# Performance work log

Measured on AMD Instinct MI355X. Metric: run time of the kernel, lower is better.

Reference implementation:

```python
import math
import jax, jax.numpy as jnp
import numpy as np

L_MAX = 3
PADDED = (1, 1, 2, 3)            # padded_l_list
K_MAX_L = (128, 96, 64, 32)      # channel bounds per l
FEATS = (32, 32, 32, 32)         # k_max_l[l] - k_max_l[l+1]
N_ATOMS = 20000
N_EDGES = 80000
N_RADIAL = 32
HIDDEN = 128
EPS = 1e-6


def setup_inputs() -> dict:
    key = jax.random.key(0)
    ks = jax.random.split(key, 40)
    it = iter(range(40))
    nk = lambda: ks[next(it)]
    inp = {}
    inp['rb'] = jax.random.normal(nk(), (L_MAX + 1, N_EDGES, N_RADIAL), jnp.float32)
    for l in range(L_MAX + 1):
        inp[f'sh{l}'] = jax.random.normal(nk(), (N_EDGES, 2 * l + 1), jnp.float32)
    for l in range(L_MAX + 1):
        P = PADDED[l]
        inp[f'f{l}'] = jax.random.normal(nk(), (N_ATOMS, P + 1, P + 1, FEATS[l]), jnp.float32)
    for P in (1, 2, 3):
        n = (P + 1) ** 2
        inp[f'U{P}'] = jax.random.normal(nk(), (n, n), jnp.float32) / math.sqrt(n)
    inp['gammas'] = jnp.ones((L_MAX + 1, 32), jnp.float32)
    inp['Win'] = jax.random.normal(nk(), (L_MAX + 1, 32, 32), jnp.float32) / math.sqrt(32.0)
    inp['Wout'] = jax.random.normal(nk(), (L_MAX + 1, 32, 32), jnp.float32) / math.sqrt(32.0)
    inp['A'] = jax.random.normal(nk(), (L_MAX + 1, N_RADIAL, HIDDEN), jnp.float32) / math.sqrt(float(N_RADIAL))
    for l in range(L_MAX + 1):
        inp[f'B{l}'] = jax.random.normal(nk(), (HIDDEN, K_MAX_L[l]), jnp.float32) / math.sqrt(float(HIDDEN))
    inp['msg_scale'] = jnp.float32(0.5)
    inp['centers'] = jax.random.randint(nk(), (N_EDGES,), 0, N_ATOMS)
    inp['neighbors'] = jax.random.randint(nk(), (N_EDGES,), 0, N_ATOMS)
    return inp


def _forward(rb, shs, feats, Us, gammas, Win, Wout, A, Bs, msg_scale, centers, neighbors):
    n_atoms = feats[0].shape[0]
    # EquivariantRMSNorm (norm over uncoupled i,j indices per channel) + linear_in
    h = []
    for l in range(L_MAX + 1):
        f = feats[l]
        rms = jnp.sqrt(jnp.mean(f * f, axis=(1, 2), keepdims=True) + EPS)
        fn = (f / rms) * gammas[l]
        h.append(jnp.einsum('nijf,fg->nijg', fn, Win[l]))
    # per-l radial MLP: [E, n_radial] -> silu -> [E, k_max_l[l]]
    rbm = [jax.nn.silu(rb[l] @ A[l]) @ Bs[l] for l in range(L_MAX + 1)]
    # vector expansion [E, 2l+1, k_max_l[l]]
    vexp = [shs[l][:, :, None] * rbm[l][:, None, :] for l in range(L_MAX + 1)]
    # split channels into per-l groups, uncouple via CG matrix U
    unc = []
    for l in range(L_MAX + 1):
        lower = K_MAX_L[l + 1] if l < L_MAX else 0
        upper = K_MAX_L[l]
        group = [vexp[lp][:, :, lower:upper] for lp in range(l + 1)]
        P = PADDED[l]
        if len(group) < P + 1:
            group.append(jnp.zeros((N_EDGES, 2 * P + 1, upper - lower), group[0].dtype))
        stacked = jnp.concatenate(group, axis=1)  # [E, (P+1)^2, feat]
        u = jnp.einsum('pq,eqf->epf', Us[P], stacked)
        unc.append(u.reshape(N_EDGES, P + 1, P + 1, upper - lower))
    # gather -> per-l tensor product -> scatter-add -> linear_out -> residual
    out = []
    for l in range(L_MAX + 1):
        P = PADDED[l]
        msg = jnp.einsum('eijf,ejkf->eikf', unc[l], h[l][neighbors]) / math.sqrt(P + 1.0)
        pooled = jnp.zeros((n_atoms,) + msg.shape[1:], msg.dtype).at[centers].add(msg) * msg_scale
        out.append(feats[l] + jnp.einsum('nijf,fg->nijg', pooled, Wout[l]))
    return tuple(out)


def reference(rb, sh0, sh1, sh2, sh3, f0, f1, f2, f3, U1, U2, U3, gammas, Win, Wout, A, B0, B1, B2, B3, msg_scale, centers, neighbors):
    return _forward(rb, [sh0, sh1, sh2, sh3], [f0, f1, f2, f3], {1: U1, 2: U2, 3: U3}, gammas, Win, Wout, A, [B0, B1, B2, B3], msg_scale, centers, neighbors)
```

## Files before the change

kernel.cpp:

```cpp
#include <hip/hip_runtime.h>
#include <cstdint>

#define NA 20000
#define NE 80000

typedef __attribute__((ext_vector_type(8))) short short8;
typedef __attribute__((ext_vector_type(4))) float f32x4;
typedef unsigned short ushort_t;

constexpr int HOFFc[4]   = {0, 2560000, 5120000, 10880000};
constexpr int RBMOFFc[4] = {0, 128, 224, 288};

__device__ __forceinline__ ushort_t f2bf(float x) {
    union { float f; unsigned u; } v; v.f = x;
    unsigned r = v.u + 0x7fffu + ((v.u >> 16) & 1u);
    return (ushort_t)(r >> 16);
}
__device__ __forceinline__ float bf2f(ushort_t u) {
    union { unsigned u; float f; } v; v.u = ((unsigned)u) << 16;
    return v.f;
}
__device__ __forceinline__ unsigned pack2(float a, float b) {
    return ((unsigned)f2bf(b) << 16) | (unsigned)f2bf(a);
}

__global__ __launch_bounds__(256)
void k_prep_w(const float* __restrict__ B0, const float* __restrict__ B1,
              const float* __restrict__ B2, const float* __restrict__ B3,
              const float* __restrict__ A, const float* __restrict__ Win,
              ushort_t* __restrict__ BT, ushort_t* __restrict__ ATb,
              ushort_t* __restrict__ WinTb)
{
    const int i = blockIdx.x * 256 + threadIdx.x;
    if (i < 40960) {
        const int n = i >> 7, k = i & 127;
        const float* src; int nl, N;
        if (n < 128)      { src = B0; nl = n;       N = 128; }
        else if (n < 224) { src = B1; nl = n - 128; N = 96;  }
        else if (n < 288) { src = B2; nl = n - 224; N = 64;  }
        else              { src = B3; nl = n - 288; N = 32;  }
        BT[i] = f2bf(src[k * N + nl]);
    } else if (i < 57344) {
        const int j2 = i - 40960;
        const int l = j2 >> 12, rem = j2 & 4095, jrow = rem >> 5, k = rem & 31;
        ATb[j2] = f2bf(A[l * 4096 + k * 128 + jrow]);
    } else if (i < 61440) {
        const int j3 = i - 57344;
        const int l = j3 >> 10, rem = j3 & 1023, g = rem >> 5, k = rem & 31;
        WinTb[j3] = f2bf(Win[l * 1024 + k * 32 + g]);
    }
}

template<int S, int AB>
__device__ __forceinline__ void norm_body(
    const float* __restrict__ fsel, const float* __restrict__ gammas, int l,
    const ushort_t* __restrict__ WinTb, ushort_t* __restrict__ hb,
    ushort_t* __restrict__ s_wt, float* __restrict__ s_scale)
{
    const int t = threadIdx.x;
    const int na0 = blockIdx.x * AB;

    if (t < 128) {
        reinterpret_cast<uint4*>(s_wt)[t] =
            reinterpret_cast<const uint4*>(WinTb + l * 1024)[t];
    }
    for (int i = t; i < AB * 32; i += 256) {
        const int a = i >> 5, c = i & 31;
        int aa = na0 + a; if (aa > NA - 1) aa = NA - 1;
        const float* fp = fsel + ((size_t)aa * S) * 32 + c;
        float ss = 0.f;
        #pragma unroll
        for (int s = 0; s < S; ++s) { const float v = fp[s * 32]; ss += v * v; }
        s_scale[i] = gammas[l * 32 + c] * rsqrtf(ss / (float)S + 1e-6f);
    }
    __syncthreads();

    const int w = t >> 6, lane = t & 63, l15 = lane & 15, lg = lane >> 4;
    const int row = w * 16 + l15;
    const bool rvalid = row < AB * S;
    const int rowc = rvalid ? row : 0;
    const int a = rowc / S, s = rowc % S;
    const int atom = na0 + a;
    const bool store_ok = rvalid && (atom < NA);
    const int atomc = (atom < NA) ? atom : (NA - 1);

    const float* fp = fsel + ((size_t)atomc * S + s) * 32 + lg * 8;
    const float4 x0 = *reinterpret_cast<const float4*>(fp);
    const float4 x1 = *reinterpret_cast<const float4*>(fp + 4);
    const float4 c0 = *reinterpret_cast<const float4*>(&s_scale[a * 32 + lg * 8]);
    const float4 c1 = *reinterpret_cast<const float4*>(&s_scale[a * 32 + lg * 8 + 4]);

    union { short8 v; unsigned u[4]; } bf;
    bf.u[0] = pack2(x0.x * c0.x, x0.y * c0.y);
    bf.u[1] = pack2(x0.z * c0.z, x0.w * c0.w);
    bf.u[2] = pack2(x1.x * c1.x, x1.y * c1.y);
    bf.u[3] = pack2(x1.z * c1.z, x1.w * c1.w);

    const short8 a0 = *reinterpret_cast<const short8*>(&s_wt[l15 * 32 + lg * 8]);
    const short8 a1 = *reinterpret_cast<const short8*>(&s_wt[(16 + l15) * 32 + lg * 8]);
    f32x4 d0 = __builtin_amdgcn_mfma_f32_16x16x32_bf16(a0, bf.v, (f32x4){0.f,0.f,0.f,0.f}, 0, 0, 0);
    f32x4 d1 = __builtin_amdgcn_mfma_f32_16x16x32_bf16(a1, bf.v, (f32x4){0.f,0.f,0.f,0.f}, 0, 0, 0);

    if (store_ok) {
        ushort_t* hp = hb + ((size_t)atomc * S + s) * 32;
        uint2 o0; o0.x = pack2(d0[0], d0[1]); o0.y = pack2(d0[2], d0[3]);
        uint2 o1; o1.x = pack2(d1[0], d1[1]); o1.y = pack2(d1[2], d1[3]);
        *reinterpret_cast<uint2*>(&hp[0  + 4 * lg]) = o0;
        *reinterpret_cast<uint2*>(&hp[16 + 4 * lg]) = o1;
    }
}

__global__ __launch_bounds__(256, 8)
void k_norm_mfma(const float* __restrict__ f0, const float* __restrict__ f1,
                 const float* __restrict__ f2, const float* __restrict__ f3,
                 const float* __restrict__ gammas, const ushort_t* __restrict__ WinTb,
                 ushort_t* __restrict__ h)
{
    __shared__ ushort_t s_wt[1024];
    __shared__ float s_scale[512];
    const int l = blockIdx.y;
    if (l == 0) {
        if (blockIdx.x >= 1250) return;
        norm_body<4, 16>(f0, gammas, 0, WinTb, h + HOFFc[0], s_wt, s_scale);
    } else if (l == 1) {
        if (blockIdx.x >= 1250) return;
        norm_body<4, 16>(f1, gammas, 1, WinTb, h + HOFFc[1], s_wt, s_scale);
    } else if (l == 2) {
        if (blockIdx.x >= 2858) return;
        norm_body<9, 7>(f2, gammas, 2, WinTb, h + HOFFc[2], s_wt, s_scale);
    } else {
        norm_body<16, 4>(f3, gammas, 3, WinTb, h + HOFFc[3], s_wt, s_scale);
    }
}

__global__ __launch_bounds__(256, 3)
void k_edgeA(const float* __restrict__ rb,
             const float* __restrict__ sh0, const float* __restrict__ sh1,
             const float* __restrict__ sh2, const float* __restrict__ sh3,
             const ushort_t* __restrict__ BT, const ushort_t* __restrict__ ATb,
             ushort_t* __restrict__ rbm, float* __restrict__ shq)
{
    __shared__ ushort_t s_h[8192];
    __shared__ ushort_t s_r2[16384];
    ushort_t* s_rbbf = s_r2;
    ushort_t* s_at   = s_r2 + 2048;
    ushort_t* s_bt   = s_r2;

    const int t  = threadIdx.x;
    const int e0 = blockIdx.x * 64;
    const int w  = t >> 6, lane = t & 63;
    const int l15 = lane & 15, lg = lane >> 4;

    for (int i = t; i < 1024; i += 256) {
        const int q = i & 15, ge = e0 + (i >> 4);
        float v;
        if (q == 0)      v = sh0[ge];
        else if (q < 4)  v = sh1[ge * 3 + (q - 1)];
        else if (q < 9)  v = sh2[ge * 5 + (q - 4)];
        else             v = sh3[ge * 7 + (q - 9)];
        shq[(size_t)e0 * 16 + i] = v;
    }

    const int Kl[4] = {128, 96, 64, 32};
    const int erow = w * 16 + l15;

    for (int l = 0; l < 4; ++l) {
        __syncthreads();
        for (int i = t; i < 1024; i += 256) {
            const float2 v = *reinterpret_cast<const float2*>(
                &rb[(size_t)l * NE * 32 + (size_t)e0 * 32 + 2 * i]);
            *reinterpret_cast<unsigned*>(&s_rbbf[2 * i]) = pack2(v.x, v.y);
        }
        {
            const uint4* src = reinterpret_cast<const uint4*>(ATb + (size_t)l * 4096);
            for (int i = t; i < 512; i += 256) reinterpret_cast<uint4*>(s_at)[i] = src[i];
        }
        __syncthreads();

        const short8 rbf = *reinterpret_cast<const short8*>(&s_rbbf[erow * 32 + lg * 8]);
        #pragma unroll
        for (int jt = 0; jt < 8; ++jt) {
            const short8 af = *reinterpret_cast<const short8*>(&s_at[(jt * 16 + l15) * 32 + lg * 8]);
            f32x4 d = __builtin_amdgcn_mfma_f32_16x16x32_bf16(af, rbf, (f32x4){0.f,0.f,0.f,0.f}, 0, 0, 0);
            float s0 = d[0] / (1.f + __expf(-d[0]));
            float s1 = d[1] / (1.f + __expf(-d[1]));
            float s2 = d[2] / (1.f + __expf(-d[2]));
            float s3 = d[3] / (1.f + __expf(-d[3]));
            const int chunk = jt * 2 + (lg >> 1);
            const int base = erow * 128 + ((chunk ^ (erow & 7)) << 3) + (lg & 1) * 4;
            uint2 ov; ov.x = pack2(s0, s1); ov.y = pack2(s2, s3);
            *reinterpret_cast<uint2*>(&s_h[base]) = ov;
        }
        __syncthreads();

        const int K = Kl[l];
        for (int cch = t; cch < (K << 4); cch += 256) {
            const int n = cch >> 4, loc = cch & 15;
            const uint4 v = *reinterpret_cast<const uint4*>(&BT[(size_t)(RBMOFFc[l] + n) * 128 + loc * 8]);
            *reinterpret_cast<uint4*>(&s_bt[n * 128 + ((loc ^ (n & 7)) << 3)]) = v;
        }
        __syncthreads();

        const short8 hf0 = *reinterpret_cast<const short8*>(&s_h[erow * 128 + (((0 + lg) ^ (erow & 7)) << 3)]);
        const short8 hf1 = *reinterpret_cast<const short8*>(&s_h[erow * 128 + (((4 + lg) ^ (erow & 7)) << 3)]);
        const short8 hf2 = *reinterpret_cast<const short8*>(&s_h[erow * 128 + (((8 + lg) ^ (erow & 7)) << 3)]);
        const short8 hf3 = *reinterpret_cast<const short8*>(&s_h[erow * 128 + (((12 + lg) ^ (erow & 7)) << 3)]);

        const int ntn = K >> 4;
        for (int nt = 0; nt < ntn; ++nt) {
            const int n = nt * 16 + l15;
            f32x4 acc = {0.f, 0.f, 0.f, 0.f};
            #pragma unroll
            for (int ks = 0; ks < 4; ++ks) {
                const short8 af = *reinterpret_cast<const short8*>(
                    &s_bt[n * 128 + (((ks * 4 + lg) ^ (n & 7)) << 3)]);
                const short8 hfk = (ks == 0) ? hf0 : (ks == 1) ? hf1 : (ks == 2) ? hf2 : hf3;
                acc = __builtin_amdgcn_mfma_f32_16x16x32_bf16(af, hfk, acc, 0, 0, 0);
            }
            uint2 ov;
            ov.x = pack2(acc[0], acc[1]);
            ov.y = pack2(acc[2], acc[3]);
            *reinterpret_cast<uint2*>(&rbm[(size_t)(e0 + erow) * 320 + RBMOFFc[l] + nt * 16 + 4 * lg]) = ov;
        }
    }
}

__global__ __launch_bounds__(256)
void k_hist(const int* __restrict__ centers, int* __restrict__ counts)
{
    const int e = blockIdx.x * 256 + threadIdx.x;
    if (e < NE) atomicAdd(&counts[centers[e]], 1);
}

__global__ __launch_bounds__(1024)
void k_scan(const int* __restrict__ counts, int* __restrict__ offsets)
{
    __shared__ int s_sum[1024];
    const int t = threadIdx.x;
    const int CH = 20;
    const int base = t * CH;
    int n = NA - base; n = n < 0 ? 0 : (n > CH ? CH : n);

    int tot = 0;
    for (int i = 0; i < n; i++) tot += counts[base + i];
    s_sum[t] = tot;
    __syncthreads();
    for (int off = 1; off < 1024; off <<= 1) {
        int v = (t >= off) ? s_sum[t - off] : 0;
        __syncthreads();
        s_sum[t] += v;
        __syncthreads();
    }
    int run = s_sum[t] - tot;
    for (int i = 0; i < n; i++) { offsets[base + i] = run; run += counts[base + i]; }
    if (t == 0) offsets[NA] = NE;
}

__global__ __launch_bounds__(256)
void k_fill(const int* __restrict__ centers, const int* __restrict__ offsets,
            int* __restrict__ cursor, int* __restrict__ elist)
{
    const int e = blockIdx.x * 256 + threadIdx.x;
    if (e < NE) {
        const int ctr = centers[e];
        const int pos = offsets[ctr] + atomicAdd(&cursor[ctr], 1);
        elist[pos] = e;
    }
}

template<int P1, int ASTART, int ACNT>
__device__ __forceinline__ void tp_step(float* __restrict__ acc,
                                        const float* __restrict__ lg,
                                        const ushort_t* __restrict__ lh,
                                        const float* __restrict__ rv, int c)
{
    float un[ACNT];
    #pragma unroll
    for (int pi = 0; pi < ACNT; ++pi) {
        const int p = ASTART + pi;
        float a = 0.f;
        #pragma unroll
        for (int lp = 0; lp < P1; ++lp) a += lg[p * 4 + lp] * rv[lp];
        un[pi] = a;
    }
    #pragma unroll
    for (int ii = 0; ii < ACNT / P1; ++ii) {
        #pragma unroll
        for (int k = 0; k < P1; ++k) {
            float m = 0.f;
            #pragma unroll
            for (int j = 0; j < P1; ++j) m += un[ii * P1 + j] * bf2f(lh[(j * P1 + k) * 32 + c]);
            acc[ii * P1 + k] += m;
        }
    }
}

template<int P1, int LOWER>
__global__ __launch_bounds__(256, 6)
void k_pool_big(const float* __restrict__ Up, float uscale,
                const float* __restrict__ WoutL, const float* __restrict__ msp,
                const float* __restrict__ shq, const ushort_t* __restrict__ rbm,
                const ushort_t* __restrict__ hL, const float* __restrict__ fL,
                float* __restrict__ outL,
                const int* __restrict__ offsets, const int* __restrict__ elist,
                const int* __restrict__ neighbors)
{
    constexpr int S       = P1 * P1;
    constexpr int ACNT0   = (P1 == 4) ? 8 : 6;
    constexpr int ACNT1   = (P1 == 4) ? 8 : 3;
    constexpr int ASTART1 = ACNT0;
    constexpr int NV      = (S * 32) / 8;

    __shared__ float    s_U[S * S];
    __shared__ float    s_w[1024];
    __shared__ ushort_t s_hbuf[4][2][S * 32];
    __shared__ float    s_gbuf[4][2][64];

    const int t = threadIdx.x;
    for (int i = t; i < S * S; i += 256) s_U[i] = Up[i] * uscale;
    for (int i = t; i < 1024; i += 256) s_w[i] = WoutL[i];
    __syncthreads();

    const int w = t >> 6, lane = t & 63, c = lane & 31, half = lane >> 5;
    const int n = blockIdx.x * 4 + w;
    const float ms = *msp;
    const int beg = offsets[n], end = offsets[n + 1];

    const int gp = lane >> 2, glp = lane & 3;
    const int qlo = (glp == 0) ? 0 : (glp == 1) ? 1 : (glp == 2) ? 4 : 9;
    const int qhi = (glp == 0) ? 1 : (glp == 1) ? 4 : (glp == 2) ? 9 : 16;
    const bool gvalid = (gp < S) && (glp < P1);

    float acc[ACNT0];
    #pragma unroll
    for (int x = 0; x < ACNT0; ++x) acc[x] = 0.f;

    ushort_t* lhA = s_hbuf[w][0];
    ushort_t* lhB = s_hbuf[w][1];
    float*    lgA = s_gbuf[w][0];
    float*    lgB = s_gbuf[w][1];

    for (int slot = beg; slot < end; slot += 2) {
        const bool haveB = (slot + 1) < end;
        const int eA = elist[slot];
        const int eB = elist[haveB ? slot + 1 : slot];
        const int nbrA = neighbors[eA];
        const int nbrB = neighbors[eB];

        uint4 vA = {}, vB = {};
        const uint4* hpA = reinterpret_cast<const uint4*>(hL + (size_t)nbrA * (S * 32));
        const uint4* hpB = reinterpret_cast<const uint4*>(hL + (size_t)nbrB * (S * 32));
        if (lane < NV) { vA = hpA[lane]; vB = hpB[lane]; }

        const ushort_t* rrA = rbm + (size_t)eA * 320 + LOWER + c;
        const ushort_t* rrB = rbm + (size_t)eB * 320 + LOWER + c;
        float rvA[4], rvB[4];
        #pragma unroll
        for (int lp = 0; lp < P1; ++lp) { rvA[lp] = bf2f(rrA[RBMOFFc[lp]]); rvB[lp] = bf2f(rrB[RBMOFFc[lp]]); }

        const float* sqA = shq + (size_t)eA * 16;
        const float* sqB = shq + (size_t)eB * 16;
        float gA = 0.f, gB = 0.f;
        if (gvalid) {
            for (int q = qlo; q < qhi; ++q) {
                const float u = s_U[gp * S + q];
                gA += u * sqA[q];
                gB += u * sqB[q];
            }
        }

        if (lane < NV) {
            reinterpret_cast<uint4*>(lhA)[lane] = vA;
            reinterpret_cast<uint4*>(lhB)[lane] = vB;
        }
        lgA[lane] = gA;
        lgB[lane] = gB;

        asm volatile("s_waitcnt lgkmcnt(0)" ::: "memory");

        if (half == 0) tp_step<P1, 0,       ACNT0>(acc, lgA, lhA, rvA, c);
        else           tp_step<P1, ASTART1, ACNT1>(acc, lgA, lhA, rvA, c);
        if (haveB) {
            if (half == 0) tp_step<P1, 0,       ACNT0>(acc, lgB, lhB, rvB, c);
            else           tp_step<P1, ASTART1, ACNT1>(acc, lgB, lhB, rvB, c);
        }
    }

    float* accStage = reinterpret_cast<float*>(s_hbuf[w]);
    if (half == 0) {
        #pragma unroll
        for (int x = 0; x < ACNT0; ++x) accStage[x * 32 + c] = acc[x];
    } else {
        #pragma unroll
        for (int x = 0; x < ACNT1; ++x) accStage[(ASTART1 + x) * 32 + c] = acc[x];
    }
    asm volatile("s_waitcnt lgkmcnt(0)" ::: "memory");

    const float* fp = fL + (size_t)n * (S * 32);
    float* op = outL + (size_t)n * (S * 32);
    for (int s = half; s < S; s += 2) {
        float o = 0.f;
        #pragma unroll
        for (int f = 0; f < 32; f++) o += accStage[s * 32 + f] * s_w[f * 32 + c];
        op[s * 32 + c] = fp[s * 32 + c] + ms * o;
    }
}

__global__ __launch_bounds__(256, 4)
void k_pool_01(const float* __restrict__ U1, const float* __restrict__ Wout,
               const float* __restrict__ msp, const float* __restrict__ shq,
               const ushort_t* __restrict__ rbm, const ushort_t* __restrict__ h,
               const float* __restrict__ f0, const float* __restrict__ f1,
               float* __restrict__ out,
               const int* __restrict__ offsets, const int* __restrict__ elist,
               const int* __restrict__ neighbors)
{
    __shared__ float s_U[16];
    __shared__ float s_w[2048];
    __shared__ float s_acc[4][2][128];

    const int t = threadIdx.x;
    if (t < 16) s_U[t] = U1[t] * 0.70710678118654752f;
    for (int i = t; i < 2048; i += 256) s_w[i] = Wout[i];
    __syncthreads();

    const int w = t >> 6, lane = t & 63, c = lane & 31, half = lane >> 5;
    const int n = blockIdx.x * 4 + w;
    const float ms = *msp;
    const int beg = offsets[n], end = offsets[n + 1];
    const ushort_t* h0 = h;
    const ushort_t* h1 = h + 2560000;

    float acc0[4] = {0.f, 0.f, 0.f, 0.f};
    float acc1[4] = {0.f, 0.f, 0.f, 0.f};

    const int nit = (end - beg + 1) >> 1;
    for (int it = 0; it < nit; ++it) {
        const int slot = beg + it * 2 + half;
        const bool valid = slot < end;
        const int e   = elist[valid ? slot : beg];
        const int nbr = neighbors[e];
        const float fac = valid ? 1.f : 0.f;

        const ushort_t* rrow = rbm + (size_t)e * 320;
        const float rv0  = fac * bf2f(rrow[96 + c]);
        const float rv1a = fac * bf2f(rrow[64 + c]);
        const float rv1b = fac * bf2f(rrow[192 + c]);
        const float* sqp = shq + (size_t)e * 16;
        const float sq0 = sqp[0], sq1 = sqp[1], sq2 = sqp[2], sq3 = sqp[3];

        float hn0[4], hn1[4];
        const ushort_t* hp0 = h0 + (size_t)nbr * 128 + c;
        const ushort_t* hp1 = h1 + (size_t)nbr * 128 + c;
        #pragma unroll
        for (int p = 0; p < 4; ++p) { hn0[p] = bf2f(hp0[p * 32]); hn1[p] = bf2f(hp1[p * 32]); }

        const float st0 = sq0 * rv0;
        float st1[4];
        st1[0] = sq0 * rv1a; st1[1] = sq1 * rv1b; st1[2] = sq2 * rv1b; st1[3] = sq3 * rv1b;

        float unc0[4], unc1[4];
        #pragma unroll
        for (int p = 0; p < 4; ++p) {
            unc0[p] = s_U[p * 4] * st0;
            float a = 0.f;
            #pragma unroll
            for (int q = 0; q < 4; ++q) a += s_U[p * 4 + q] * st1[q];
            unc1[p] = a;
        }
        #pragma unroll
        for (int i = 0; i < 2; ++i) {
            #pragma unroll
            for (int k = 0; k < 2; ++k) {
                float m0 = 0.f, m1 = 0.f;
                #pragma unroll
                for (int j = 0; j < 2; ++j) {
                    m0 += unc0[i * 2 + j] * hn0[j * 2 + k];
                    m1 += unc1[i * 2 + j] * hn1[j * 2 + k];
                }
                acc0[i * 2 + k] += m0;
                acc1[i * 2 + k] += m1;
            }
        }
    }

    #pragma unroll
    for (int s = 0; s < 4; s++) { acc0[s] += __shfl_xor(acc0[s], 32); acc1[s] += __shfl_xor(acc1[s], 32); }
    #pragma unroll
    for (int s = 0; s < 4; s++) if ((s & 1) == half) {
        s_acc[w][0][s * 32 + c] = acc0[s];
        s_acc[w][1][s * 32 + c] = acc1[s];
    }
    __syncthreads();

    const float* fp0 = f0 + (size_t)n * 128;
    const float* fp1 = f1 + (size_t)n * 128;
    float* op0 = out + (size_t)n * 128;
    float* op1 = out + 2560000 + (size_t)n * 128;
    for (int s = half; s < 4; s += 2) {
        float o0 = 0.f, o1 = 0.f;
        #pragma unroll
        for (int f = 0; f < 32; f++) {
            o0 += s_acc[w][0][s * 32 + f] * s_w[f * 32 + c];
            o1 += s_acc[w][1][s * 32 + f] * s_w[1024 + f * 32 + c];
        }
        op0[s * 32 + c] = fp0[s * 32 + c] + ms * o0;
        op1[s * 32 + c] = fp1[s * 32 + c] + ms * o1;
    }
}

extern "C" void kernel_launch(void* const* d_in, const int* in_sizes, int n_in,
                              void* d_out, int out_size, void* d_ws, size_t ws_size,
                              hipStream_t stream)
{
    (void)in_sizes; (void)n_in; (void)out_size;

    const float* rb     = (const float*)d_in[0];
    const float* sh0    = (const float*)d_in[1];
    const float* sh1    = (const float*)d_in[2];
    const float* sh2    = (const float*)d_in[3];
    const float* sh3    = (const float*)d_in[4];
    const float* f0     = (const float*)d_in[5];
    const float* f1     = (const float*)d_in[6];
    const float* f2     = (const float*)d_in[7];
    const float* f3     = (const float*)d_in[8];
    const float* U1     = (const float*)d_in[9];
    const float* U2     = (const float*)d_in[10];
    const float* U3     = (const float*)d_in[11];
    const float* gammas = (const float*)d_in[12];
    const float* Win    = (const float*)d_in[13];
    const float* Wout   = (const float*)d_in[14];
    const float* A      = (const float*)d_in[15];
    const float* B0     = (const float*)d_in[16];
    const float* B1     = (const float*)d_in[17];
    const float* B2     = (const float*)d_in[18];
    const float* B3     = (const float*)d_in[19];
    const float* msp    = (const float*)d_in[20];
    const int* centers   = (const int*)d_in[21];
    const int* neighbors = (const int*)d_in[22];

    const size_t OFF_RBM = 42240000;
    const size_t OFF_SHQ = 93440000;
    const size_t OFF_BT  = 98560000;
    const size_t OFF_AT  = 98641920;
    const size_t OFF_WT  = 98674688;
    const size_t OFF_INT = 98682880;
    const size_t needed  = OFF_INT + (size_t)140001 * 4;
    if (ws_size < needed) return;

    ushort_t* h_bf  = (ushort_t*)d_ws;
    ushort_t* rbm   = (ushort_t*)((char*)d_ws + OFF_RBM);
    float*    shq   = (float*)((char*)d_ws + OFF_SHQ);
    ushort_t* BT    = (ushort_t*)((char*)d_ws + OFF_BT);
    ushort_t* ATb   = (ushort_t*)((char*)d_ws + OFF_AT);
    ushort_t* WinTb = (ushort_t*)((char*)d_ws + OFF_WT);
    int* ibase   = (int*)((char*)d_ws + OFF_INT);
    int* offsets = ibase;
    int* counts  = ibase + 20001;
    int* cursor  = ibase + 40001;
    int* elist   = ibase + 60001;

    hipMemsetAsync(counts, 0, (size_t)40000 * sizeof(int), stream);

    k_hist<<<313, 256, 0, stream>>>(centers, counts);
    k_scan<<<1, 1024, 0, stream>>>(counts, offsets);
    k_fill<<<313, 256, 0, stream>>>(centers, offsets, cursor, elist);
    k_prep_w<<<240, 256, 0, stream>>>(B0, B1, B2, B3, A, Win, BT, ATb, WinTb);

    dim3 gN(5000, 4);
    k_norm_mfma<<<gN, 256, 0, stream>>>(f0, f1, f2, f3, gammas, WinTb, h_bf);
    k_edgeA<<<1250, 256, 0, stream>>>(rb, sh0, sh1, sh2, sh3, BT, ATb, rbm, shq);

    float* out = (float*)d_out;
    k_pool_01<<<5000, 256, 0, stream>>>(U1, Wout, msp, shq, rbm, h_bf, f0, f1, out,
                                        offsets, elist, neighbors);
    k_pool_big<3, 32><<<5000, 256, 0, stream>>>(U2, 0.57735026918962576f, Wout + 2048, msp,
                                                shq, rbm, h_bf + HOFFc[2], f2, out + HOFFc[2],
                                                offsets, elist, neighbors);
    k_pool_big<4, 0><<<5000, 256, 0, stream>>>(U3, 0.5f, Wout + 3072, msp,
                                               shq, rbm, h_bf + HOFFc[3], f3, out + HOFFc[3],
                                               offsets, elist, neighbors);
}
```

Before: 316.4 us.

## Fuse per-l pooling kernels into one and split edge MLP across l blocks

Replaces the three pooling kernels (l=0/1 combined, l=2, l=3) with a single kernel that walks each atom's edge list once and accumulates every l. Each edge's index, neighbor, rbm row and shq values are therefore loaded once instead of three times. The edge MLP kernel now uses a 2D grid with one block per (edge tile, l) instead of looping over l inside a block, which gives more blocks and fewer barriers per block. In exchange, the fused pool kernel holds more registers and shared memory per block, drops the two-edge software pipelining, and processes edges one at a time with more work per iteration.

```diff
diff --git a/kernel.cpp b/kernel.cpp
--- a/kernel.cpp
+++ b/kernel.cpp
@@ -148,80 +148,80 @@
 
     const int t  = threadIdx.x;
     const int e0 = blockIdx.x * 64;
+    const int l  = blockIdx.y;
     const int w  = t >> 6, lane = t & 63;
     const int l15 = lane & 15, lg = lane >> 4;
 
-    for (int i = t; i < 1024; i += 256) {
-        const int q = i & 15, ge = e0 + (i >> 4);
-        float v;
-        if (q == 0)      v = sh0[ge];
-        else if (q < 4)  v = sh1[ge * 3 + (q - 1)];
-        else if (q < 9)  v = sh2[ge * 5 + (q - 4)];
-        else             v = sh3[ge * 7 + (q - 9)];
-        shq[(size_t)e0 * 16 + i] = v;
+    if (l == 0) {
+        for (int i = t; i < 1024; i += 256) {
+            const int q = i & 15, ge = e0 + (i >> 4);
+            float v;
+            if (q == 0)      v = sh0[ge];
+            else if (q < 4)  v = sh1[ge * 3 + (q - 1)];
+            else if (q < 9)  v = sh2[ge * 5 + (q - 4)];
+            else             v = sh3[ge * 7 + (q - 9)];
+            shq[(size_t)e0 * 16 + i] = v;
+        }
     }
 
     const int Kl[4] = {128, 96, 64, 32};
     const int erow = w * 16 + l15;
 
-    for (int l = 0; l < 4; ++l) {
-        __syncthreads();
-        for (int i = t; i < 1024; i += 256) {
-            const float2 v = *reinterpret_cast<const float2*>(
-                &rb[(size_t)l * NE * 32 + (size_t)e0 * 32 + 2 * i]);
-            *reinterpret_cast<unsigned*>(&s_rbbf[2 * i]) = pack2(v.x, v.y);
+    for (int i = t; i < 1024; i += 256) {
+        const float2 v = *reinterpret_cast<const float2*>(
+            &rb[(size_t)l * NE * 32 + (size_t)e0 * 32 + 2 * i]);
+        *reinterpret_cast<unsigned*>(&s_rbbf[2 * i]) = pack2(v.x, v.y);
+    }
+    {
+        const uint4* src = reinterpret_cast<const uint4*>(ATb + (size_t)l * 4096);
+        for (int i = t; i < 512; i += 256) reinterpret_cast<uint4*>(s_at)[i] = src[i];
+    }
+    __syncthreads();
+
+    const short8 rbf = *reinterpret_cast<const short8*>(&s_rbbf[erow * 32 + lg * 8]);
+    #pragma unroll
+    for (int jt = 0; jt < 8; ++jt) {
+        const short8 af = *reinterpret_cast<const short8*>(&s_at[(jt * 16 + l15) * 32 + lg * 8]);
+        f32x4 d = __builtin_amdgcn_mfma_f32_16x16x32_bf16(af, rbf, (f32x4){0.f,0.f,0.f,0.f}, 0, 0, 0);
+        float s0 = d[0] / (1.f + __expf(-d[0]));
+        float s1 = d[1] / (1.f + __expf(-d[1]));
+        float s2 = d[2] / (1.f + __expf(-d[2]));
+        float s3 = d[3] / (1.f + __expf(-d[3]));
+        const int chunk = jt * 2 + (lg >> 1);
+        const int base = erow * 128 + ((chunk ^ (erow & 7)) << 3) + (lg & 1) * 4;
+        uint2 ov; ov.x = pack2(s0, s1); ov.y = pack2(s2, s3);
+        *reinterpret_cast<uint2*>(&s_h[base]) = ov;
+    }
+    __syncthreads();
+
+    const int K = Kl[l];
+    for (int cch = t; cch < (K << 4); cch += 256) {
+        const int n = cch >> 4, loc = cch & 15;
+        const uint4 v = *reinterpret_cast<const uint4*>(&BT[(size_t)(RBMOFFc[l] + n) * 128 + loc * 8]);
+        *reinterpret_cast<uint4*>(&s_bt[n * 128 + ((loc ^ (n & 7)) << 3)]) = v;
+    }
+    __syncthreads();
+
+    const short8 hf0 = *reinterpret_cast<const short8*>(&s_h[erow * 128 + (((0 + lg) ^ (erow & 7)) << 3)]);
+    const short8 hf1 = *reinterpret_cast<const short8*>(&s_h[erow * 128 + (((4 + lg) ^ (erow & 7)) << 3)]);
+    const short8 hf2 = *reinterpret_cast<const short8*>(&s_h[erow * 128 + (((8 + lg) ^ (erow & 7)) << 3)]);
+    const short8 hf3 = *reinterpret_cast<const short8*>(&s_h[erow * 128 + (((12 + lg) ^ (erow & 7)) << 3)]);
+
+    const int ntn = K >> 4;
+    for (int nt = 0; nt < ntn; ++nt) {
+        const int n = nt * 16 + l15;
+        f32x4 acc = {0.f, 0.f, 0.f, 0.f};
+        #pragma unroll
+        for (int ks = 0; ks < 4; ++ks) {
+            const short8 af = *reinterpret_cast<const short8*>(
+                &s_bt[n * 128 + (((ks * 4 + lg) ^ (n & 7)) << 3)]);
+            const short8 hfk = (ks == 0) ? hf0 : (ks == 1) ? hf1 : (ks == 2) ? hf2 : hf3;
+            acc = __builtin_amdgcn_mfma_f32_16x16x32_bf16(af, hfk, acc, 0, 0, 0);
         }
-        {
-            const uint4* src = reinterpret_cast<const uint4*>(ATb + (size_t)l * 4096);
-            for (int i = t; i < 512; i += 256) reinterpret_cast<uint4*>(s_at)[i] = src[i];
-        }
-        __syncthreads();
-
-        const short8 rbf = *reinterpret_cast<const short8*>(&s_rbbf[erow * 32 + lg * 8]);
-        #pragma unroll
-        for (int jt = 0; jt < 8; ++jt) {
-            const short8 af = *reinterpret_cast<const short8*>(&s_at[(jt * 16 + l15) * 32 + lg * 8]);
-            f32x4 d = __builtin_amdgcn_mfma_f32_16x16x32_bf16(af, rbf, (f32x4){0.f,0.f,0.f,0.f}, 0, 0, 0);
-            float s0 = d[0] / (1.f + __expf(-d[0]));
-            float s1 = d[1] / (1.f + __expf(-d[1]));
-            float s2 = d[2] / (1.f + __expf(-d[2]));
-            float s3 = d[3] / (1.f + __expf(-d[3]));
-            const int chunk = jt * 2 + (lg >> 1);
-            const int base = erow * 128 + ((chunk ^ (erow & 7)) << 3) + (lg & 1) * 4;
-            uint2 ov; ov.x = pack2(s0, s1); ov.y = pack2(s2, s3);
-            *reinterpret_cast<uint2*>(&s_h[base]) = ov;
-        }
-        __syncthreads();
-
-        const int K = Kl[l];
-        for (int cch = t; cch < (K << 4); cch += 256) {
-            const int n = cch >> 4, loc = cch & 15;
-            const uint4 v = *reinterpret_cast<const uint4*>(&BT[(size_t)(RBMOFFc[l] + n) * 128 + loc * 8]);
-            *reinterpret_cast<uint4*>(&s_bt[n * 128 + ((loc ^ (n & 7)) << 3)]) = v;
-        }
-        __syncthreads();
-
-        const short8 hf0 = *reinterpret_cast<const short8*>(&s_h[erow * 128 + (((0 + lg) ^ (erow & 7)) << 3)]);
-        const short8 hf1 = *reinterpret_cast<const short8*>(&s_h[erow * 128 + (((4 + lg) ^ (erow & 7)) << 3)]);
-        const short8 hf2 = *reinterpret_cast<const short8*>(&s_h[erow * 128 + (((8 + lg) ^ (erow & 7)) << 3)]);
-        const short8 hf3 = *reinterpret_cast<const short8*>(&s_h[erow * 128 + (((12 + lg) ^ (erow & 7)) << 3)]);
-
-        const int ntn = K >> 4;
-        for (int nt = 0; nt < ntn; ++nt) {
-            const int n = nt * 16 + l15;
-            f32x4 acc = {0.f, 0.f, 0.f, 0.f};
-            #pragma unroll
-            for (int ks = 0; ks < 4; ++ks) {
-                const short8 af = *reinterpret_cast<const short8*>(
-                    &s_bt[n * 128 + (((ks * 4 + lg) ^ (n & 7)) << 3)]);
-                const short8 hfk = (ks == 0) ? hf0 : (ks == 1) ? hf1 : (ks == 2) ? hf2 : hf3;
-                acc = __builtin_amdgcn_mfma_f32_16x16x32_bf16(af, hfk, acc, 0, 0, 0);
-            }
-            uint2 ov;
-            ov.x = pack2(acc[0], acc[1]);
-            ov.y = pack2(acc[2], acc[3]);
-            *reinterpret_cast<uint2*>(&rbm[(size_t)(e0 + erow) * 320 + RBMOFFc[l] + nt * 16 + 4 * lg]) = ov;
-        }
+        uint2 ov;
+        ov.x = pack2(acc[0], acc[1]);
+        ov.y = pack2(acc[2], acc[3]);
+        *reinterpret_cast<uint2*>(&rbm[(size_t)(e0 + erow) * 320 + RBMOFFc[l] + nt * 16 + 4 * lg]) = ov;
     }
 }
 
@@ -295,30 +295,43 @@
     }
 }
 
-template<int P1, int LOWER>
-__global__ __launch_bounds__(256, 6)
-void k_pool_big(const float* __restrict__ Up, float uscale,
-                const float* __restrict__ WoutL, const float* __restrict__ msp,
-                const float* __restrict__ shq, const ushort_t* __restrict__ rbm,
-                const ushort_t* __restrict__ hL, const float* __restrict__ fL,
-                float* __restrict__ outL,
+template<int S>
+__device__ __forceinline__ void ep_out(const float* __restrict__ ab,
+                                       const float* __restrict__ sw,
+                                       const float* __restrict__ fp,
+                                       float* __restrict__ op,
+                                       float ms, int c, int half)
+{
+    for (int s = half; s < S; s += 2) {
+        float o = 0.f;
+        #pragma unroll
+        for (int f = 0; f < 32; ++f) o += ab[s * 32 + f] * sw[f * 32 + c];
+        op[s * 32 + c] = fp[s * 32 + c] + ms * o;
+    }
+}
+
+__global__ __launch_bounds__(256, 4)
+void k_pool_all(const float* __restrict__ U1, const float* __restrict__ U2,
+                const float* __restrict__ U3, const float* __restrict__ Wout,
+                const float* __restrict__ msp, const float* __restrict__ shq,
+                const ushort_t* __restrict__ rbm, const ushort_t* __restrict__ h,
+                const float* __restrict__ f0, const float* __restrict__ f1,
+                const float* __restrict__ f2, const float* __restrict__ f3,
+                float* __restrict__ out,
                 const int* __restrict__ offsets, const int* __restrict__ elist,
                 const int* __restrict__ neighbors)
 {
-    constexpr int S       = P1 * P1;
-    constexpr int ACNT0   = (P1 == 4) ? 8 : 6;
-    constexpr int ACNT1   = (P1 == 4) ? 8 : 3;
-    constexpr int ASTART1 = ACNT0;
-    constexpr int NV      = (S * 32) / 8;
-
-    __shared__ float    s_U[S * S];
-    __shared__ float    s_w[1024];
-    __shared__ ushort_t s_hbuf[4][2][S * 32];
-    __shared__ float    s_gbuf[4][2][64];
+    __shared__ float s_w[4096];
+    __shared__ float s_U3[256];
+    __shared__ float s_U2[81];
+    __shared__ float s_U1[16];
+    __shared__ float s_wb[4][1056];
 
     const int t = threadIdx.x;
-    for (int i = t; i < S * S; i += 256) s_U[i] = Up[i] * uscale;
-    for (int i = t; i < 1024; i += 256) s_w[i] = WoutL[i];
+    for (int i = t; i < 4096; i += 256) s_w[i] = Wout[i];
+    if (t < 256) s_U3[t] = U3[t] * 0.5f;
+    if (t < 81)  s_U2[t] = U2[t] * 0.57735026918962576f;
+    if (t < 16)  s_U1[t] = U1[t] * 0.70710678118654752f;
     __syncthreads();
 
     const int w = t >> 6, lane = t & 63, c = lane & 31, half = lane >> 5;
@@ -329,184 +342,109 @@
     const int gp = lane >> 2, glp = lane & 3;
     const int qlo = (glp == 0) ? 0 : (glp == 1) ? 1 : (glp == 2) ? 4 : 9;
     const int qhi = (glp == 0) ? 1 : (glp == 1) ? 4 : (glp == 2) ? 9 : 16;
-    const bool gvalid = (gp < S) && (glp < P1);
-
-    float acc[ACNT0];
-    #pragma unroll
-    for (int x = 0; x < ACNT0; ++x) acc[x] = 0.f;
-
-    ushort_t* lhA = s_hbuf[w][0];
-    ushort_t* lhB = s_hbuf[w][1];
-    float*    lgA = s_gbuf[w][0];
-    float*    lgB = s_gbuf[w][1];
-
-    for (int slot = beg; slot < end; slot += 2) {
-        const bool haveB = (slot + 1) < end;
-        const int eA = elist[slot];
-        const int eB = elist[haveB ? slot + 1 : slot];
-        const int nbrA = neighbors[eA];
-        const int nbrB = neighbors[eB];
-
-        uint4 vA = {}, vB = {};
-        const uint4* hpA = reinterpret_cast<const uint4*>(hL + (size_t)nbrA * (S * 32));
-        const uint4* hpB = reinterpret_cast<const uint4*>(hL + (size_t)nbrB * (S * 32));
-        if (lane < NV) { vA = hpA[lane]; vB = hpB[lane]; }
-
-        const ushort_t* rrA = rbm + (size_t)eA * 320 + LOWER + c;
-        const ushort_t* rrB = rbm + (size_t)eB * 320 + LOWER + c;
-        float rvA[4], rvB[4];
-        #pragma unroll
-        for (int lp = 0; lp < P1; ++lp) { rvA[lp] = bf2f(rrA[RBMOFFc[lp]]); rvB[lp] = bf2f(rrB[RBMOFFc[lp]]); }
-
-        const float* sqA = shq + (size_t)eA * 16;
-        const float* sqB = shq + (size_t)eB * 16;
-        float gA = 0.f, gB = 0.f;
-        if (gvalid) {
-            for (int q = qlo; q < qhi; ++q) {
-                const float u = s_U[gp * S + q];
-                gA += u * sqA[q];
-                gB += u * sqB[q];
-            }
-        }
-
-        if (lane < NV) {
-            reinterpret_cast<uint4*>(lhA)[lane] = vA;
-            reinterpret_cast<uint4*>(lhB)[lane] = vB;
-        }
-        lgA[lane] = gA;
-        lgB[lane] = gB;
-
-        asm volatile("s_waitcnt lgkmcnt(0)" ::: "memory");
-
-        if (half == 0) tp_step<P1, 0,       ACNT0>(acc, lgA, lhA, rvA, c);
-        else           tp_step<P1, ASTART1, ACNT1>(acc, lgA, lhA, rvA, c);
-        if (haveB) {
-            if (half == 0) tp_step<P1, 0,       ACNT0>(acc, lgB, lhB, rvB, c);
-            else           tp_step<P1, ASTART1, ACNT1>(acc, lgB, lhB, rvB, c);
-        }
-    }
-
-    float* accStage = reinterpret_cast<float*>(s_hbuf[w]);
-    if (half == 0) {
-        #pragma unroll
-        for (int x = 0; x < ACNT0; ++x) accStage[x * 32 + c] = acc[x];
-    } else {
-        #pragma unroll
-        for (int x = 0; x < ACNT1; ++x) accStage[(ASTART1 + x) * 32 + c] = acc[x];
-    }
-    asm volatile("s_waitcnt lgkmcnt(0)" ::: "memory");
-
-    const float* fp = fL + (size_t)n * (S * 32);
-    float* op = outL + (size_t)n * (S * 32);
-    for (int s = half; s < S; s += 2) {
-        float o = 0.f;
-        #pragma unroll
-        for (int f = 0; f < 32; f++) o += accStage[s * 32 + f] * s_w[f * 32 + c];
-        op[s * 32 + c] = fp[s * 32 + c] + ms * o;
-    }
-}
-
-__global__ __launch_bounds__(256, 4)
-void k_pool_01(const float* __restrict__ U1, const float* __restrict__ Wout,
-               const float* __restrict__ msp, const float* __restrict__ shq,
-               const ushort_t* __restrict__ rbm, const ushort_t* __restrict__ h,
-               const float* __restrict__ f0, const float* __restrict__ f1,
-               float* __restrict__ out,
-               const int* __restrict__ offsets, const int* __restrict__ elist,
-               const int* __restrict__ neighbors)
-{
-    __shared__ float s_U[16];
-    __shared__ float s_w[2048];
-    __shared__ float s_acc[4][2][128];
-
-    const int t = threadIdx.x;
-    if (t < 16) s_U[t] = U1[t] * 0.70710678118654752f;
-    for (int i = t; i < 2048; i += 256) s_w[i] = Wout[i];
-    __syncthreads();
-
-    const int w = t >> 6, lane = t & 63, c = lane & 31, half = lane >> 5;
-    const int n = blockIdx.x * 4 + w;
-    const float ms = *msp;
-    const int beg = offsets[n], end = offsets[n + 1];
-    const ushort_t* h0 = h;
-    const ushort_t* h1 = h + 2560000;
-
-    float acc0[4] = {0.f, 0.f, 0.f, 0.f};
-    float acc1[4] = {0.f, 0.f, 0.f, 0.f};
-
-    const int nit = (end - beg + 1) >> 1;
-    for (int it = 0; it < nit; ++it) {
-        const int slot = beg + it * 2 + half;
-        const bool valid = slot < end;
-        const int e   = elist[valid ? slot : beg];
+    const bool g2v = (gp < 9) && (glp < 3);
+
+    ushort_t* lh3 = reinterpret_cast<ushort_t*>(s_wb[w]);
+    ushort_t* lh2 = lh3 + 512;
+    float* lg3 = s_wb[w] + 400;
+    float* lg2 = s_wb[w] + 464;
+
+    const ushort_t* h0 = h + HOFFc[0];
+    const ushort_t* h1 = h + HOFFc[1];
+    const ushort_t* h2 = h + HOFFc[2];
+    const ushort_t* h3 = h + HOFFc[3];
+
+    float acc3[8] = {0.f,0.f,0.f,0.f,0.f,0.f,0.f,0.f};
+    float acc2[6] = {0.f,0.f,0.f,0.f,0.f,0.f};
+    float a00 = 0.f, a01 = 0.f, a10 = 0.f, a11 = 0.f;
+
+    for (int slot = beg; slot < end; ++slot) {
+        const int e   = elist[slot];
         const int nbr = neighbors[e];
-        const float fac = valid ? 1.f : 0.f;
+
+        const uint4* hp3 = reinterpret_cast<const uint4*>(h3 + (size_t)nbr * 512);
+        const uint4* hp2 = reinterpret_cast<const uint4*>(h2 + (size_t)nbr * 288);
+        uint4 v3 = hp3[lane];
+        uint4 v2 = {};
+        if (lane < 36) v2 = hp2[lane];
+
+        const ushort_t* hq0 = h0 + (size_t)nbr * 128 + c;
+        const ushort_t* hq1 = h1 + (size_t)nbr * 128 + c;
+        const float hn0_0 = bf2f(hq0[0]),  hn0_1 = bf2f(hq0[32]);
+        const float hn0_2 = bf2f(hq0[64]), hn0_3 = bf2f(hq0[96]);
+        const float hn1_0 = bf2f(hq1[0]),  hn1_1 = bf2f(hq1[32]);
+        const float hn1_2 = bf2f(hq1[64]), hn1_3 = bf2f(hq1[96]);
 
         const ushort_t* rrow = rbm + (size_t)e * 320;
-        const float rv0  = fac * bf2f(rrow[96 + c]);
-        const float rv1a = fac * bf2f(rrow[64 + c]);
-        const float rv1b = fac * bf2f(rrow[192 + c]);
+        const float r0   = bf2f(rrow[96 + c]);
+        const float r1a  = bf2f(rrow[64 + c]),  r1b  = bf2f(rrow[192 + c]);
+        float rv2[3];
+        rv2[0] = bf2f(rrow[32 + c]); rv2[1] = bf2f(rrow[160 + c]); rv2[2] = bf2f(rrow[256 + c]);
+        float rv3[4];
+        rv3[0] = bf2f(rrow[0 + c]);  rv3[1] = bf2f(rrow[128 + c]);
+        rv3[2] = bf2f(rrow[224 + c]); rv3[3] = bf2f(rrow[288 + c]);
+
         const float* sqp = shq + (size_t)e * 16;
         const float sq0 = sqp[0], sq1 = sqp[1], sq2 = sqp[2], sq3 = sqp[3];
 
-        float hn0[4], hn1[4];
-        const ushort_t* hp0 = h0 + (size_t)nbr * 128 + c;
-        const ushort_t* hp1 = h1 + (size_t)nbr * 128 + c;
-        #pragma unroll
-        for (int p = 0; p < 4; ++p) { hn0[p] = bf2f(hp0[p * 32]); hn1[p] = bf2f(hp1[p * 32]); }
-
-        const float st0 = sq0 * rv0;
-        float st1[4];
-        st1[0] = sq0 * rv1a; st1[1] = sq1 * rv1b; st1[2] = sq2 * rv1b; st1[3] = sq3 * rv1b;
-
-        float unc0[4], unc1[4];
-        #pragma unroll
-        for (int p = 0; p < 4; ++p) {
-            unc0[p] = s_U[p * 4] * st0;
-            float a = 0.f;
-            #pragma unroll
-            for (int q = 0; q < 4; ++q) a += s_U[p * 4 + q] * st1[q];
-            unc1[p] = a;
+        float g3 = 0.f;
+        for (int q = qlo; q < qhi; ++q) g3 += s_U3[gp * 16 + q] * sqp[q];
+        float g2 = 0.f;
+        if (g2v) { for (int q = qlo; q < qhi; ++q) g2 += s_U2[gp * 9 + q] * sqp[q]; }
+
+        reinterpret_cast<uint4*>(lh3)[lane] = v3;
+        if (lane < 36) reinterpret_cast<uint4*>(lh2)[lane] = v2;
+        lg3[lane] = g3;
+        if (lane < 36) lg2[lane] = g2;
+
+        asm volatile("s_waitcnt lgkmcnt(0)" ::: "memory");
+
+        if (half == 0) {
+            tp_step<4, 0, 8>(acc3, lg3, lh3, rv3, c);
+            tp_step<3, 0, 6>(acc2, lg2, lh2, rv2, c);
+        } else {
+            tp_step<4, 8, 8>(acc3, lg3, lh3, rv3, c);
+            tp_step<3, 6, 3>(acc2, lg2, lh2, rv2, c);
         }
-        #pragma unroll
-        for (int i = 0; i < 2; ++i) {
-            #pragma unroll
-            for (int k = 0; k < 2; ++k) {
-                float m0 = 0.f, m1 = 0.f;
-                #pragma unroll
-                for (int j = 0; j < 2; ++j) {
-                    m0 += unc0[i * 2 + j] * hn0[j * 2 + k];
-                    m1 += unc1[i * 2 + j] * hn1[j * 2 + k];
-                }
-                acc0[i * 2 + k] += m0;
-                acc1[i * 2 + k] += m1;
-            }
-        }
-    }
-
-    #pragma unroll
-    for (int s = 0; s < 4; s++) { acc0[s] += __shfl_xor(acc0[s], 32); acc1[s] += __shfl_xor(acc1[s], 32); }
-    #pragma unroll
-    for (int s = 0; s < 4; s++) if ((s & 1) == half) {
-        s_acc[w][0][s * 32 + c] = acc0[s];
-        s_acc[w][1][s * 32 + c] = acc1[s];
-    }
-    __syncthreads();
-
-    const float* fp0 = f0 + (size_t)n * 128;
-    const float* fp1 = f1 + (size_t)n * 128;
-    float* op0 = out + (size_t)n * 128;
-    float* op1 = out + 2560000 + (size_t)n * 128;
-    for (int s = half; s < 4; s += 2) {
-        float o0 = 0.f, o1 = 0.f;
-        #pragma unroll
-        for (int f = 0; f < 32; f++) {
-            o0 += s_acc[w][0][s * 32 + f] * s_w[f * 32 + c];
-            o1 += s_acc[w][1][s * 32 + f] * s_w[1024 + f * 32 + c];
-        }
-        op0[s * 32 + c] = fp0[s * 32 + c] + ms * o0;
-        op1[s * 32 + c] = fp1[s * 32 + c] + ms * o1;
-    }
+
+        const float st0   = sq0 * r0;
+        const float st1_0 = sq0 * r1a, st1_1 = sq1 * r1b, st1_2 = sq2 * r1b, st1_3 = sq3 * r1b;
+        const int i2 = half * 2;
+        const float u0_0 = s_U1[(i2 + 0) * 4] * st0;
+        const float u0_1 = s_U1[(i2 + 1) * 4] * st0;
+        const float u1_0 = s_U1[(i2+0)*4+0]*st1_0 + s_U1[(i2+0)*4+1]*st1_1 + s_U1[(i2+0)*4+2]*st1_2 + s_U1[(i2+0)*4+3]*st1_3;
+        const float u1_1 = s_U1[(i2+1)*4+0]*st1_0 + s_U1[(i2+1)*4+1]*st1_1 + s_U1[(i2+1)*4+2]*st1_2 + s_U1[(i2+1)*4+3]*st1_3;
+        a00 += u0_0 * hn0_0 + u0_1 * hn0_2;
+        a01 += u0_0 * hn0_1 + u0_1 * hn0_3;
+        a10 += u1_0 * hn1_0 + u1_1 * hn1_2;
+        a11 += u1_0 * hn1_1 + u1_1 * hn1_3;
+    }
+
+    asm volatile("s_waitcnt lgkmcnt(0)" ::: "memory");
+
+    float* ab = s_wb[w];
+    ab[0   + (half * 2 + 0) * 32 + c] = a00;
+    ab[0   + (half * 2 + 1) * 32 + c] = a01;
+    ab[128 + (half * 2 + 0) * 32 + c] = a10;
+    ab[128 + (half * 2 + 1) * 32 + c] = a11;
+    if (half == 0) {
+        #pragma unroll
+        for (int x = 0; x < 6; ++x) ab[256 + x * 32 + c] = acc2[x];
+        #pragma unroll
+        for (int x = 0; x < 8; ++x) ab[544 + x * 32 + c] = acc3[x];
+    } else {
+        #pragma unroll
+        for (int x = 0; x < 3; ++x) ab[256 + (6 + x) * 32 + c] = acc2[x];
+        #pragma unroll
+        for (int x = 0; x < 8; ++x) ab[544 + (8 + x) * 32 + c] = acc3[x];
+    }
+    asm volatile("s_waitcnt lgkmcnt(0)" ::: "memory");
+
+    const float ms_ = ms;
+    ep_out<4>(ab,        s_w,        f0 + (size_t)n * 128, out + HOFFc[0] + (size_t)n * 128, ms_, c, half);
+    ep_out<4>(ab + 128,  s_w + 1024, f1 + (size_t)n * 128, out + HOFFc[1] + (size_t)n * 128, ms_, c, half);
+    ep_out<9>(ab + 256,  s_w + 2048, f2 + (size_t)n * 288, out + HOFFc[2] + (size_t)n * 288, ms_, c, half);
+    ep_out<16>(ab + 544, s_w + 3072, f3 + (size_t)n * 512, out + HOFFc[3] + (size_t)n * 512, ms_, c, half);
 }
 
 extern "C" void kernel_launch(void* const* d_in, const int* in_sizes, int n_in,
@@ -569,15 +507,10 @@
 
     dim3 gN(5000, 4);
     k_norm_mfma<<<gN, 256, 0, stream>>>(f0, f1, f2, f3, gammas, WinTb, h_bf);
-    k_edgeA<<<1250, 256, 0, stream>>>(rb, sh0, sh1, sh2, sh3, BT, ATb, rbm, shq);
-
-    float* out = (float*)d_out;
-    k_pool_01<<<5000, 256, 0, stream>>>(U1, Wout, msp, shq, rbm, h_bf, f0, f1, out,
-                                        offsets, elist, neighbors);
-    k_pool_big<3, 32><<<5000, 256, 0, stream>>>(U2, 0.57735026918962576f, Wout + 2048, msp,
-                                                shq, rbm, h_bf + HOFFc[2], f2, out + HOFFc[2],
-                                                offsets, elist, neighbors);
-    k_pool_big<4, 0><<<5000, 256, 0, stream>>>(U3, 0.5f, Wout + 3072, msp,
-                                               shq, rbm, h_bf + HOFFc[3], f3, out + HOFFc[3],
-                                               offsets, elist, neighbors);
-}
+    dim3 gE(1250, 4);
+    k_edgeA<<<gE, 256, 0, stream>>>(rb, sh0, sh1, sh2, sh3, BT, ATb, rbm, shq);
+
+    k_pool_all<<<5000, 256, 0, stream>>>(U1, U2, U3, Wout, msp, shq, rbm, h_bf,
+                                         f0, f1, f2, f3, (float*)d_out,
+                                         offsets, elist, neighbors);
+}
```

Result: slower. 368.2 us (+16.4%).
